# Performance work log

Measured on AMD Instinct MI355X. Metric: run time of the kernel, lower is better.

The kernel has to match this reference:

```python
import jax, jax.numpy as jnp
import numpy as np

K = 8
WRM = 40


def _gru(x, h, w_ih, w_hh, b_ih, b_hh):
    # PyTorch GRU cell: gates ordered (r, z, n)
    gi = x @ w_ih.T + b_ih
    gh = h @ w_hh.T + b_hh
    i_r, i_z, i_n = jnp.split(gi, 3, axis=-1)
    h_r, h_z, h_n = jnp.split(gh, 3, axis=-1)
    r = jax.nn.sigmoid(i_r + h_r)
    z = jax.nn.sigmoid(i_z + h_z)
    n = jnp.tanh(i_n + r * h_n)
    return (1.0 - z) * n + z * h


def setup_inputs() -> dict:
    key = jax.random.key(0)
    ks = jax.random.split(key, 20)
    T, B, C, Wd, H = 240, 64, 1, 84, 84
    N, M, E, A = 512, 256, 32, 18
    D = C * Wd * H
    u = lambda k, s, sc: jax.random.uniform(k, s, jnp.float32, -sc, sc)
    sM = float(1.0 / np.sqrt(M))
    sD = float(1.0 / np.sqrt(D))
    return dict(
        obs_seq=jax.random.normal(ks[0], (T, B, C, Wd, H), jnp.float32),
        act_seq=jax.random.randint(ks[1], (T, B), 0, A),
        w_enc=u(ks[2], (N, D), sD), b_enc=u(ks[3], (N,), sD),
        w_ih=u(ks[4], (3 * M, N), sM), w_hh=u(ks[5], (3 * M, M), sM),
        b_ih=u(ks[6], (3 * M,), sM), b_hh=u(ks[7], (3 * M,), sM),
        w_ih_c=u(ks[8], (3 * M, E), sM), w_hh_c=u(ks[9], (3 * M, M), sM),
        b_ih_c=u(ks[10], (3 * M,), sM), b_hh_c=u(ks[11], (3 * M,), sM),
        W1=u(ks[12], (M, M), sM), b1=u(ks[13], (M,), sM),
        W2=u(ks[14], (N, M), sM), b2=u(ks[15], (N,), sM),
        emb=jax.random.normal(ks[16], (A, E), jnp.float32),
    )


def reference(obs_seq, act_seq, w_enc, b_enc, w_ih, w_hh, b_ih, b_hh,
              w_ih_c, w_hh_c, b_ih_c, b_hh_c, W1, b1, W2, b2, emb):
    T, B = obs_seq.shape[0], obs_seq.shape[1]
    M = w_hh.shape[1]
    # encoder: flatten + linear -> (T, B, N)
    z = obs_seq.reshape(T, B, -1) @ w_enc.T + b_enc
    wrm_seq, trn_seq = z[:WRM], z[WRM:]
    acts = act_seq[WRM:]

    h0 = jnp.zeros((B, M), z.dtype)
    warm_hn, _ = jax.lax.scan(
        lambda h, x: (_gru(x, h, w_ih, w_hh, b_ih, b_hh), None), h0, wrm_seq)
    warm_hn = jax.lax.stop_gradient(warm_hn)  # torch.no_grad() warmup

    def cls_step(h, x):
        h2 = _gru(x, h, w_ih, w_hh, b_ih, b_hh)
        return h2, h2

    _, bts = jax.lax.scan(cls_step, warm_hn, trn_seq)  # (T', B, M)

    Tp = bts.shape[0]
    Tout = Tp - K
    idx = jnp.arange(Tout)[:, None] + jnp.arange(K)[None, :]  # (Tout, K)
    act_win = emb[acts[idx]]  # (Tout, K, B, E)

    def open_step(h, x):  # h: (Tout, B, M), x: (Tout, B, E)
        h2 = _gru(x, h, w_ih_c, w_hh_c, b_ih_c, b_hh_c)
        zt = jax.nn.relu(h2 @ W1.T + b1) @ W2.T + b2
        return h2, zt

    _, zs = jax.lax.scan(open_step, bts[:Tout], jnp.transpose(act_win, (1, 0, 2, 3)))
    return jnp.transpose(zs, (1, 0, 2, 3))  # (Tout, K, B, N)
```

## Files before the change

kernel.cpp:

```cpp
#include <hip/hip_runtime.h>
#include <hip/hip_fp16.h>
#include <math.h>

#define TT   240
#define BBATCH 64
#define DDIM 7056
#define KENC_PAD 7072
#define NENC 512
#define MHID 256
#define G3   768
#define WRMC 40
#define KWIN 8
#define TOUTC 192
#define RROWS (TOUTC*BBATCH)
#define NSTEPS (WRMC + TOUTC)

#define B_GI     ((size_t)0)
#define B_WENCH  ((size_t)0)
#define B_GBH    ((size_t)0)
#define B_R1H    ((size_t)37748736)
#define B_ZH     ((size_t)45613056)
#define B_HOPEN  ((size_t)45613056)
#define B_BTS    ((size_t)60817408)
#define B_BTSH   ((size_t)73400320)
#define B_HOPENH ((size_t)79691776)
#define B_WIHH   ((size_t)85983232)
#define B_WHHCH  ((size_t)86769664)
#define B_W1H    ((size_t)87162880)
#define B_W2H    ((size_t)87293952)
#define B_GTAB   ((size_t)87556096)
#define B_WT8    ((size_t)87611392)

typedef _Float16 half8 __attribute__((ext_vector_type(8)));
typedef _Float16 h2v  __attribute__((ext_vector_type(2)));
typedef __attribute__((ext_vector_type(4))) float f32x4;

__device__ __forceinline__ float sigmf(float x) { return 1.0f / (1.0f + expf(-x)); }
__device__ __forceinline__ h2v u2h2(unsigned int u) {
  union { unsigned int u; h2v h; } c; c.u = u; return c.h;
}

__global__ void wconv_kernel(const float* __restrict__ W, __half* __restrict__ o,
                             int N, int K, int Kpad) {
  const int idx = blockIdx.x * 256 + threadIdx.x;
  if (idx >= N * Kpad) return;
  const int n = idx / Kpad, k = idx % Kpad;
  o[idx] = __float2half((k < K) ? W[(size_t)n * K + k] : 0.f);
}

template<int AF32>
__global__ __launch_bounds__(256, 3) void gemm_hp(
    const void* __restrict__ A, const __half* __restrict__ W,
    const float* __restrict__ bias, void* __restrict__ C,
    int M, int N, int K, int Kpad, int relu, int out_h, int outk)
{
  __shared__ __half Ah[2][64][40];
  __shared__ __half Bh[2][256][40];
  const int tid = threadIdx.x;
  const int bx = blockIdx.x, by = blockIdx.y;
  const int w = tid >> 6;
  const int lane = tid & 63;
  const int l15 = lane & 15;
  const int khalf = (lane >> 4) * 8;
  const int arow = tid >> 2;
  const int akq = (tid & 3) * 8;
  const int bn = tid >> 2, bk = (tid & 3) * 8;

  f32x4 acc[4][4];
#pragma unroll
  for (int i = 0; i < 4; ++i)
#pragma unroll
    for (int j = 0; j < 4; ++j) acc[i][j] = (f32x4){0.f, 0.f, 0.f, 0.f};

  const int niter = Kpad / 32;

  float4 raA0, raA1, rahA, rbA0, rbA1, rbA2, rbA3;
  float4 raB0, raB1, rahB, rbB0, rbB1, rbB2, rbB3;

#define LOADT(IT, ra0, ra1, rah, rb0, rb1, rb2, rb3)                              \
  {                                                                               \
    const int k0_ = (IT) * 32;                                                    \
    if (AF32) {                                                                   \
      const float* Af_ = (const float*)A;                                         \
      ra0 = make_float4(0.f, 0.f, 0.f, 0.f); ra1 = ra0;                           \
      const size_t base_ = (size_t)(by * 64 + arow) * K + k0_ + akq;              \
      if (k0_ + akq < K)     ra0 = *(const float4*)(Af_ + base_);                 \
      if (k0_ + akq + 4 < K) ra1 = *(const float4*)(Af_ + base_ + 4);             \
    } else {                                                                      \
      rah = *(const float4*)((const __half*)A +                                   \
            (size_t)(by * 64 + arow) * Kpad + k0_ + akq);                         \
    }                                                                             \
    rb0 = *(const float4*)(W + (size_t)(bx * 256 + bn      ) * Kpad + k0_ + bk);  \
    rb1 = *(const float4*)(W + (size_t)(bx * 256 + bn +  64) * Kpad + k0_ + bk);  \
    rb2 = *(const float4*)(W + (size_t)(bx * 256 + bn + 128) * Kpad + k0_ + bk);  \
    rb3 = *(const float4*)(W + (size_t)(bx * 256 + bn + 192) * Kpad + k0_ + bk);  \
  }

#define BODY(IT, ra0, ra1, rah, rb0, rb1, rb2, rb3)                               \
  {                                                                               \
    __half (*Ac)[40] = Ah[(IT) & 1];                                              \
    __half (*Bc)[40] = Bh[(IT) & 1];                                              \
    if (AF32) {                                                                   \
      __half2 hh_[4];                                                             \
      hh_[0] = __floats2half2_rn(ra0.x, ra0.y);                                   \
      hh_[1] = __floats2half2_rn(ra0.z, ra0.w);                                   \
      hh_[2] = __floats2half2_rn(ra1.x, ra1.y);                                   \
      hh_[3] = __floats2half2_rn(ra1.z, ra1.w);                                   \
      *(float4*)&Ac[arow][akq] = *(float4*)hh_;                                   \
    } else {                                                                      \
      *(float4*)&Ac[arow][akq] = rah;                                             \
    }                                                                             \
    *(float4*)&Bc[bn      ][bk] = rb0;                                            \
    *(float4*)&Bc[bn +  64][bk] = rb1;                                            \
    *(float4*)&Bc[bn + 128][bk] = rb2;                                            \
    *(float4*)&Bc[bn + 192][bk] = rb3;                                            \
    __syncthreads();                                                              \
    if ((IT) + 2 < niter)                                                         \
      LOADT((IT) + 2, ra0, ra1, rah, rb0, rb1, rb2, rb3);                         \
    half8 ah_[4], bh_[4];                                                         \
    _Pragma("unroll")                                                             \
    for (int i = 0; i < 4; ++i) ah_[i] = *(half8*)&Ac[i * 16 + l15][khalf];       \
    _Pragma("unroll")                                                             \
    for (int j = 0; j < 4; ++j) bh_[j] = *(half8*)&Bc[w * 64 + j * 16 + l15][khalf]; \
    _Pragma("unroll")                                                             \
    for (int i = 0; i < 4; ++i)                                                   \
      _Pragma("unroll")                                                           \
      for (int j = 0; j < 4; ++j)                                                 \
        acc[i][j] = __builtin_amdgcn_mfma_f32_16x16x32_f16(ah_[i], bh_[j], acc[i][j], 0, 0, 0); \
  }

  LOADT(0, raA0, raA1, rahA, rbA0, rbA1, rbA2, rbA3);
  if (niter > 1) LOADT(1, raB0, raB1, rahB, rbB0, rbB1, rbB2, rbB3);

  int it = 0;
  while (true) {
    BODY(it, raA0, raA1, rahA, rbA0, rbA1, rbA2, rbA3);
    ++it; if (it == niter) break;
    BODY(it, raB0, raB1, rahB, rbB0, rbB1, rbB2, rbB3);
    ++it; if (it == niter) break;
  }
#undef BODY
#undef LOADT

  const int r4 = (lane >> 4) * 4;
#pragma unroll
  for (int j = 0; j < 4; ++j) {
    const int col = bx * 256 + w * 64 + j * 16 + l15;
    const float bc = bias ? bias[col] : 0.f;
#pragma unroll
    for (int i = 0; i < 4; ++i) {
      const int mbase = by * 64 + i * 16 + r4;
#pragma unroll
      for (int r = 0; r < 4; ++r) {
        const int m = mbase + r;
        float vv = acc[i][j][r] + bc;
        if (relu) vv = fmaxf(vv, 0.f);
        if (outk >= 0) {
          const int t = m >> 6, b = m & 63;
          ((float*)C)[(((size_t)(t * KWIN + outk) * BBATCH + b) * NENC) + col] = vv;
        } else if (out_h) {
          ((__half*)C)[(size_t)m * N + col] = __float2half(vv);
        } else {
          ((float*)C)[(size_t)m * N + col] = vv;
        }
      }
    }
  }
}

__global__ void gitab_kernel(const float* __restrict__ emb, const float* __restrict__ w_ih_c,
                             const float* __restrict__ b_ih_c, float* __restrict__ gt)
{
  const int idx = blockIdx.x * blockDim.x + threadIdx.x;
  if (idx >= 18 * G3) return;
  const int a = idx / G3, cgate = idx % G3;
  float s = b_ih_c[cgate];
#pragma unroll
  for (int e = 0; e < 32; ++e) s = fmaf(emb[a * 32 + e], w_ih_c[cgate * 32 + e], s);
  gt[idx] = s;
}

__global__ void transpose_whh_p8(const float* __restrict__ w, float4* __restrict__ wt8) {
  const int id = blockIdx.x * 256 + threadIdx.x;
  if (id >= 32 * G3) return;
  const int k8 = id / G3, j = id % G3;
  const float* src = w + (size_t)j * MHID + k8 * 8;
  __half2 h2[4];
#pragma unroll
  for (int q = 0; q < 4; ++q)
    h2[q] = __floats2half2_rn(src[2 * q], src[2 * q + 1]);
  wt8[id] = *(float4*)h2;
}

__global__ __launch_bounds__(768, 3) void scan4_kernel(
    const float* __restrict__ gi_all, const float4* __restrict__ wt8,
    const float* __restrict__ b_hh, float* __restrict__ bts,
    __half* __restrict__ bts_h)
{
  const int b = blockIdx.x;
  const int j = threadIdx.x;
  __shared__ __align__(16) float hs[256];
  __shared__ __align__(16) __half hs16[256];
  __shared__ float gacc[768];

  unsigned int wreg[128];
#pragma unroll
  for (int k8 = 0; k8 < 32; ++k8) {
    const float4 v = wt8[(size_t)k8 * G3 + j];
    const uint4 u = *(const uint4*)&v;
    wreg[k8 * 4 + 0] = u.x; wreg[k8 * 4 + 1] = u.y;
    wreg[k8 * 4 + 2] = u.z; wreg[k8 * 4 + 3] = u.w;
  }
  const float bj = b_hh[j];
  if (j < 256) { hs[j] = 0.f; hs16[j] = __float2half(0.f); }
  __syncthreads();

  const uint4* h16v = (const uint4*)hs16;

  for (int t = 0; t < NSTEPS; ++t) {
    float gr = 0.f, gz = 0.f, gn = 0.f;
    if (j < 256) {
      const float* gp = gi_all + ((size_t)t * BBATCH + b) * G3;
      gr = gp[j]; gz = gp[256 + j]; gn = gp[512 + j];
    }

    float a0 = bj, a1 = 0.f, a2 = 0.f, a3 = 0.f;
#pragma unroll
    for (int k8 = 0; k8 < 32; ++k8) {
      const uint4 hu = h16v[k8];
#if __has_builtin(__builtin_amdgcn_fdot2)
      a0 = __builtin_amdgcn_fdot2(u2h2(wreg[k8 * 4 + 0]), u2h2(hu.x), a0, false);
      a1 = __builtin_amdgcn_fdot2(u2h2(wreg[k8 * 4 + 1]), u2h2(hu.y), a1, false);
      a2 = __builtin_amdgcn_fdot2(u2h2(wreg[k8 * 4 + 2]), u2h2(hu.z), a2, false);
      a3 = __builtin_amdgcn_fdot2(u2h2(wreg[k8 * 4 + 3]), u2h2(hu.w), a3, false);
#else
      {
        const h2v w0 = u2h2(wreg[k8 * 4 + 0]), w1 = u2h2(wreg[k8 * 4 + 1]);
        const h2v w2 = u2h2(wreg[k8 * 4 + 2]), w3 = u2h2(wreg[k8 * 4 + 3]);
        const h2v x0 = u2h2(hu.x), x1 = u2h2(hu.y), x2 = u2h2(hu.z), x3 = u2h2(hu.w);
        a0 = fmaf((float)w0.x, (float)x0.x, a0); a0 = fmaf((float)w0.y, (float)x0.y, a0);
        a1 = fmaf((float)w1.x, (float)x1.x, a1); a1 = fmaf((float)w1.y, (float)x1.y, a1);
        a2 = fmaf((float)w2.x, (float)x2.x, a2); a2 = fmaf((float)w2.y, (float)x2.y, a2);
        a3 = fmaf((float)w3.x, (float)x3.x, a3); a3 = fmaf((float)w3.y, (float)x3.y, a3);
      }
#endif
    }
    gacc[j] = (a0 + a1) + (a2 + a3);
    __syncthreads();

    if (j < 256) {
      const float r = sigmf(gr + gacc[j]);
      const float z = sigmf(gz + gacc[256 + j]);
      const float n = tanhf(gn + r * gacc[512 + j]);
      const float hn = (1.f - z) * n + z * hs[j];
      hs[j] = hn;
      hs16[j] = __float2half(hn);
      if (t >= WRMC) {
        const size_t o = (((size_t)(t - WRMC)) * BBATCH + b) * MHID + j;
        bts[o] = hn;
        bts_h[o] = __float2half(hn);
      }
    }
    __syncthreads();
  }
}

__global__ __launch_bounds__(256) void open_gates(
    const float* __restrict__ gtab, const int* __restrict__ act_seq,
    const float* __restrict__ gh, const float* __restrict__ hin,
    float* __restrict__ hout, __half* __restrict__ hout_h, int kstep)
{
  const int row = blockIdx.x;
  const int j = threadIdx.x;
  const int t = row >> 6, b = row & 63;
  const int a = act_seq[(WRMC + t + kstep) * BBATCH + b];
  const float* gi = gtab + a * G3;
  const float gr = gi[j], gz = gi[256 + j], gn = gi[512 + j];
  const size_t g0 = (size_t)row * G3;
  const float hr = gh[g0 + j], hz = gh[g0 + 256 + j], hnn = gh[g0 + 512 + j];
  const float h = hin[(size_t)row * MHID + j];
  const float r = sigmf(gr + hr);
  const float z = sigmf(gz + hz);
  const float n = tanhf(gn + r * hnn);
  const float hn = (1.f - z) * n + z * h;
  hout[(size_t)row * MHID + j] = hn;
  hout_h[(size_t)row * MHID + j] = __float2half(hn);
}

extern "C" void kernel_launch(void* const* d_in, const int* in_sizes, int n_in,
                              void* d_out, int out_size, void* d_ws, size_t ws_size,
                              hipStream_t stream) {
  const float* obs    = (const float*)d_in[0];
  const int*   act    = (const int*)  d_in[1];
  const float* w_enc  = (const float*)d_in[2];
  const float* b_enc  = (const float*)d_in[3];
  const float* w_ih   = (const float*)d_in[4];
  const float* w_hh   = (const float*)d_in[5];
  const float* b_ih   = (const float*)d_in[6];
  const float* b_hh   = (const float*)d_in[7];
  const float* w_ih_c = (const float*)d_in[8];
  const float* w_hh_c = (const float*)d_in[9];
  const float* b_ih_c = (const float*)d_in[10];
  const float* b_hh_c = (const float*)d_in[11];
  const float* W1     = (const float*)d_in[12];
  const float* b1     = (const float*)d_in[13];
  const float* W2     = (const float*)d_in[14];
  const float* b2     = (const float*)d_in[15];
  const float* emb    = (const float*)d_in[16];

  char* wsb = (char*)d_ws;
  float* out = (float*)d_out;

  float*  gi      = (float*)(wsb + B_GI);
  float*  gbh     = (float*)(wsb + B_GBH);
  __half* r1_h    = (__half*)(wsb + B_R1H);
  __half* z_h     = (__half*)(wsb + B_ZH);
  float*  hopen   = (float*)(wsb + B_HOPEN);
  float*  bts     = (float*)(wsb + B_BTS);
  __half* bts_h   = (__half*)(wsb + B_BTSH);
  __half* hopen_h = (__half*)(wsb + B_HOPENH);
  __half* enc_h   = (__half*)(wsb + B_WENCH);
  __half* ih_h    = (__half*)(wsb + B_WIHH);
  __half* hhc_h   = (__half*)(wsb + B_WHHCH);
  __half* w1_h    = (__half*)(wsb + B_W1H);
  __half* w2_h    = (__half*)(wsb + B_W2H);
  float*  gtab    = (float*)(wsb + B_GTAB);
  float4* wt8     = (float4*)(wsb + B_WT8);

  const dim3 blk(256);

  wconv_kernel<<<(NENC * KENC_PAD + 255) / 256, blk, 0, stream>>>(w_enc, enc_h, NENC, DDIM, KENC_PAD);
  wconv_kernel<<<(G3 * NENC + 255) / 256, blk, 0, stream>>>(w_ih, ih_h, G3, NENC, NENC);
  wconv_kernel<<<(G3 * MHID + 255) / 256, blk, 0, stream>>>(w_hh_c, hhc_h, G3, MHID, MHID);
  wconv_kernel<<<(MHID * MHID + 255) / 256, blk, 0, stream>>>(W1, w1_h, MHID, MHID, MHID);
  wconv_kernel<<<(NENC * MHID + 255) / 256, blk, 0, stream>>>(W2, w2_h, NENC, MHID, MHID);
  gitab_kernel<<<54, 256, 0, stream>>>(emb, w_ih_c, b_ih_c, gtab);
  transpose_whh_p8<<<(32 * G3 + 255) / 256, blk, 0, stream>>>(w_hh, wt8);

  gemm_hp<1><<<dim3(NENC / 256, NSTEPS * BBATCH / 64), blk, 0, stream>>>(
      obs, enc_h, b_enc, z_h, NSTEPS * BBATCH, NENC, DDIM, KENC_PAD, 0, 1, -1);
  gemm_hp<0><<<dim3(G3 / 256, NSTEPS * BBATCH / 64), blk, 0, stream>>>(
      z_h, ih_h, b_ih, gi, NSTEPS * BBATCH, G3, NENC, NENC, 0, 0, -1);

  scan4_kernel<<<BBATCH, 768, 0, stream>>>(gi, wt8, b_hh, bts, bts_h);

  for (int k = 0; k < KWIN; ++k) {
    const __half* hin_h = (k == 0) ? bts_h : hopen_h;
    const float*  hin   = (k == 0) ? bts   : hopen;
    gemm_hp<0><<<dim3(G3 / 256, RROWS / 64), blk, 0, stream>>>(
        hin_h, hhc_h, b_hh_c, gbh, RROWS, G3, MHID, MHID, 0, 0, -1);
    open_gates<<<RROWS, 256, 0, stream>>>(gtab, act, gbh, hin, hopen, hopen_h, k);
    gemm_hp<0><<<dim3(MHID / 256, RROWS / 64), blk, 0, stream>>>(
        hopen_h, w1_h, b1, r1_h, RROWS, MHID, MHID, MHID, 1, 1, -1);
    gemm_hp<0><<<dim3(NENC / 256, RROWS / 64), blk, 0, stream>>>(
        r1_h, w2_h, b2, out, RROWS, NENC, MHID, MHID, 0, 0, k);
  }
}
```

Baseline: 1.104 ms.

## Fuse the 8-step open-loop GRU and MLP into one per-timestep kernel

Replaces the per-step sequence of four launches (hidden GEMM, gate kernel, W1 GEMM, W2 GEMM) across 8 open-loop steps with a single kernel. Each block handles one time index for all 64 batch rows and keeps hidden state in registers and LDS across the 8 steps, using MFMA directly with weights read from global memory. This removes about 32 launches and the global round-trips of gate, hidden and relu intermediates. In exchange it launches only 192 blocks of 512 threads with a large LDS footprint, rounds gate pre-activations to fp16, and rereads weights from global without LDS staging.

Result: slower. 1.384 ms (+25.3%).

```diff
diff --git a/kernel.cpp b/kernel.cpp
--- a/kernel.cpp
+++ b/kernel.cpp
@@ -17,13 +17,8 @@
 
 #define B_GI     ((size_t)0)
 #define B_WENCH  ((size_t)0)
-#define B_GBH    ((size_t)0)
-#define B_R1H    ((size_t)37748736)
 #define B_ZH     ((size_t)45613056)
-#define B_HOPEN  ((size_t)45613056)
 #define B_BTS    ((size_t)60817408)
-#define B_BTSH   ((size_t)73400320)
-#define B_HOPENH ((size_t)79691776)
 #define B_WIHH   ((size_t)85983232)
 #define B_WHHCH  ((size_t)86769664)
 #define B_W1H    ((size_t)87162880)
@@ -52,7 +47,7 @@
 __global__ __launch_bounds__(256, 3) void gemm_hp(
     const void* __restrict__ A, const __half* __restrict__ W,
     const float* __restrict__ bias, void* __restrict__ C,
-    int M, int N, int K, int Kpad, int relu, int out_h, int outk)
+    int M, int N, int K, int Kpad, int relu, int out_h)
 {
   __shared__ __half Ah[2][64][40];
   __shared__ __half Bh[2][256][40];
@@ -155,14 +150,8 @@
         const int m = mbase + r;
         float vv = acc[i][j][r] + bc;
         if (relu) vv = fmaxf(vv, 0.f);
-        if (outk >= 0) {
-          const int t = m >> 6, b = m & 63;
-          ((float*)C)[(((size_t)(t * KWIN + outk) * BBATCH + b) * NENC) + col] = vv;
-        } else if (out_h) {
-          ((__half*)C)[(size_t)m * N + col] = __float2half(vv);
-        } else {
-          ((float*)C)[(size_t)m * N + col] = vv;
-        }
+        if (out_h) ((__half*)C)[(size_t)m * N + col] = __float2half(vv);
+        else       ((float*)C)[(size_t)m * N + col] = vv;
       }
     }
   }
@@ -194,8 +183,7 @@
 
 __global__ __launch_bounds__(768, 3) void scan4_kernel(
     const float* __restrict__ gi_all, const float4* __restrict__ wt8,
-    const float* __restrict__ b_hh, float* __restrict__ bts,
-    __half* __restrict__ bts_h)
+    const float* __restrict__ b_hh, float* __restrict__ bts)
 {
   const int b = blockIdx.x;
   const int j = threadIdx.x;
@@ -255,36 +243,191 @@
       const float hn = (1.f - z) * n + z * hs[j];
       hs[j] = hn;
       hs16[j] = __float2half(hn);
-      if (t >= WRMC) {
-        const size_t o = (((size_t)(t - WRMC)) * BBATCH + b) * MHID + j;
-        bts[o] = hn;
-        bts_h[o] = __float2half(hn);
-      }
-    }
-    __syncthreads();
-  }
-}
-
-__global__ __launch_bounds__(256) void open_gates(
+      if (t >= WRMC) bts[(((size_t)(t - WRMC)) * BBATCH + b) * MHID + j] = hn;
+    }
+    __syncthreads();
+  }
+}
+
+__global__ __launch_bounds__(512, 2) void open8_kernel(
+    const float* __restrict__ bts,
+    const __half* __restrict__ whhc, const float* __restrict__ bhhc,
+    const __half* __restrict__ w1, const float* __restrict__ b1v,
+    const __half* __restrict__ w2, const float* __restrict__ b2v,
     const float* __restrict__ gtab, const int* __restrict__ act_seq,
-    const float* __restrict__ gh, const float* __restrict__ hin,
-    float* __restrict__ hout, __half* __restrict__ hout_h, int kstep)
+    float* __restrict__ out)
 {
-  const int row = blockIdx.x;
-  const int j = threadIdx.x;
-  const int t = row >> 6, b = row & 63;
-  const int a = act_seq[(WRMC + t + kstep) * BBATCH + b];
-  const float* gi = gtab + a * G3;
-  const float gr = gi[j], gz = gi[256 + j], gn = gi[512 + j];
-  const size_t g0 = (size_t)row * G3;
-  const float hr = gh[g0 + j], hz = gh[g0 + 256 + j], hnn = gh[g0 + 512 + j];
-  const float h = hin[(size_t)row * MHID + j];
-  const float r = sigmf(gr + hr);
-  const float z = sigmf(gz + hz);
-  const float n = tanhf(gn + r * hnn);
-  const float hn = (1.f - z) * n + z * h;
-  hout[(size_t)row * MHID + j] = hn;
-  hout_h[(size_t)row * MHID + j] = __float2half(hn);
+  __shared__ __align__(16) __half h16s[64][264];
+  __shared__ __align__(16) __half gbuf[768 * 68];
+  __shared__ int a_lds[64];
+
+  const int t = blockIdx.x;
+  const int tid = threadIdx.x;
+  const int w = tid >> 6;
+  const int lane = tid & 63;
+  const int l15 = lane & 15;
+  const int khalf = (lane >> 4) * 8;
+  const int r4 = (lane >> 4) * 4;
+  const int grow = tid & 63;
+  const int jb = tid >> 6;
+
+  float h32[32];
+  {
+    const float* src = bts + ((size_t)t * 64 + grow) * 256 + jb * 32;
+#pragma unroll
+    for (int q = 0; q < 8; ++q) {
+      const float4 v = *(const float4*)(src + q * 4);
+      h32[q * 4 + 0] = v.x; h32[q * 4 + 1] = v.y;
+      h32[q * 4 + 2] = v.z; h32[q * 4 + 3] = v.w;
+    }
+#pragma unroll
+    for (int q = 0; q < 4; ++q) {
+      __half2 hh[4];
+#pragma unroll
+      for (int p = 0; p < 4; ++p)
+        hh[p] = __floats2half2_rn(h32[q * 8 + p * 2], h32[q * 8 + p * 2 + 1]);
+      *(float4*)&h16s[grow][jb * 32 + q * 8] = *(float4*)hh;
+    }
+  }
+  __syncthreads();
+
+  for (int k = 0; k < KWIN; ++k) {
+    if (tid < 64) a_lds[tid] = act_seq[(WRMC + t + k) * BBATCH + tid];
+
+    f32x4 accG[4][6];
+#pragma unroll
+    for (int m = 0; m < 4; ++m)
+#pragma unroll
+      for (int c = 0; c < 6; ++c) accG[m][c] = (f32x4){0.f, 0.f, 0.f, 0.f};
+#pragma unroll
+    for (int kf = 0; kf < 8; ++kf) {
+      half8 ah[4];
+#pragma unroll
+      for (int m = 0; m < 4; ++m)
+        ah[m] = *(const half8*)&h16s[m * 16 + l15][kf * 32 + khalf];
+#pragma unroll
+      for (int c = 0; c < 6; ++c) {
+        const int col = (w * 6 + c) * 16 + l15;
+        const half8 bf = *(const half8*)(whhc + (size_t)col * 256 + kf * 32 + khalf);
+#pragma unroll
+        for (int m = 0; m < 4; ++m)
+          accG[m][c] = __builtin_amdgcn_mfma_f32_16x16x32_f16(ah[m], bf, accG[m][c], 0, 0, 0);
+      }
+    }
+#pragma unroll
+    for (int c = 0; c < 6; ++c) {
+      const int col = (w * 6 + c) * 16 + l15;
+#pragma unroll
+      for (int m = 0; m < 4; ++m) {
+        const int row0 = m * 16 + r4;
+        short4 s;
+        s.x = __half_as_short(__float2half(accG[m][c][0]));
+        s.y = __half_as_short(__float2half(accG[m][c][1]));
+        s.z = __half_as_short(__float2half(accG[m][c][2]));
+        s.w = __half_as_short(__float2half(accG[m][c][3]));
+        *(short4*)&gbuf[col * 68 + row0] = s;
+      }
+    }
+    __syncthreads();
+
+    {
+      const int a = a_lds[grow];
+      const float* gt = gtab + (size_t)a * G3;
+#pragma unroll
+      for (int i = 0; i < 32; ++i) {
+        const int col = jb * 32 + i;
+        const float ghR = __half2float(gbuf[(col)*68 + grow]);
+        const float ghZ = __half2float(gbuf[(col + 256) * 68 + grow]);
+        const float ghN = __half2float(gbuf[(col + 512) * 68 + grow]);
+        const float rr = sigmf(gt[col] + ghR + bhhc[col]);
+        const float zz = sigmf(gt[col + 256] + ghZ + bhhc[col + 256]);
+        const float nn = tanhf(gt[col + 512] + rr * (ghN + bhhc[col + 512]));
+        h32[i] = (1.f - zz) * nn + zz * h32[i];
+      }
+#pragma unroll
+      for (int q = 0; q < 4; ++q) {
+        __half2 hh[4];
+#pragma unroll
+        for (int p = 0; p < 4; ++p)
+          hh[p] = __floats2half2_rn(h32[q * 8 + p * 2], h32[q * 8 + p * 2 + 1]);
+        *(float4*)&h16s[grow][jb * 32 + q * 8] = *(float4*)hh;
+      }
+    }
+    __syncthreads();
+
+    f32x4 accT[4][2];
+#pragma unroll
+    for (int m = 0; m < 4; ++m)
+#pragma unroll
+      for (int c = 0; c < 2; ++c) accT[m][c] = (f32x4){0.f, 0.f, 0.f, 0.f};
+#pragma unroll
+    for (int kf = 0; kf < 8; ++kf) {
+      half8 ah[4];
+#pragma unroll
+      for (int m = 0; m < 4; ++m)
+        ah[m] = *(const half8*)&h16s[m * 16 + l15][kf * 32 + khalf];
+#pragma unroll
+      for (int c = 0; c < 2; ++c) {
+        const int col = (w * 2 + c) * 16 + l15;
+        const half8 bf = *(const half8*)(w1 + (size_t)col * 256 + kf * 32 + khalf);
+#pragma unroll
+        for (int m = 0; m < 4; ++m)
+          accT[m][c] = __builtin_amdgcn_mfma_f32_16x16x32_f16(ah[m], bf, accT[m][c], 0, 0, 0);
+      }
+    }
+    {
+      __half (*t1p)[264] = (__half(*)[264])gbuf;
+#pragma unroll
+      for (int c = 0; c < 2; ++c) {
+        const int col = (w * 2 + c) * 16 + l15;
+        const float bb = b1v[col];
+#pragma unroll
+        for (int m = 0; m < 4; ++m)
+#pragma unroll
+          for (int q = 0; q < 4; ++q)
+            t1p[m * 16 + r4 + q][col] = __float2half(fmaxf(accT[m][c][q] + bb, 0.f));
+      }
+    }
+    __syncthreads();
+
+    f32x4 accO[4][4];
+#pragma unroll
+    for (int m = 0; m < 4; ++m)
+#pragma unroll
+      for (int c = 0; c < 4; ++c) accO[m][c] = (f32x4){0.f, 0.f, 0.f, 0.f};
+    {
+      __half (*t1p)[264] = (__half(*)[264])gbuf;
+#pragma unroll
+      for (int kf = 0; kf < 8; ++kf) {
+        half8 ah[4];
+#pragma unroll
+        for (int m = 0; m < 4; ++m)
+          ah[m] = *(const half8*)&t1p[m * 16 + l15][kf * 32 + khalf];
+#pragma unroll
+        for (int c = 0; c < 4; ++c) {
+          const int col = (w * 4 + c) * 16 + l15;
+          const half8 bf = *(const half8*)(w2 + (size_t)col * 256 + kf * 32 + khalf);
+#pragma unroll
+          for (int m = 0; m < 4; ++m)
+            accO[m][c] = __builtin_amdgcn_mfma_f32_16x16x32_f16(ah[m], bf, accO[m][c], 0, 0, 0);
+        }
+      }
+    }
+    {
+      const size_t obase = (size_t)(t * KWIN + k) * BBATCH;
+#pragma unroll
+      for (int c = 0; c < 4; ++c) {
+        const int col = (w * 4 + c) * 16 + l15;
+        const float bb = b2v[col];
+#pragma unroll
+        for (int m = 0; m < 4; ++m)
+#pragma unroll
+          for (int q = 0; q < 4; ++q)
+            out[(obase + m * 16 + r4 + q) * NENC + col] = accO[m][c][q] + bb;
+      }
+    }
+    __syncthreads();
+  }
 }
 
 extern "C" void kernel_launch(void* const* d_in, const int* in_sizes, int n_in,
@@ -311,21 +454,16 @@
   char* wsb = (char*)d_ws;
   float* out = (float*)d_out;
 
-  float*  gi      = (float*)(wsb + B_GI);
-  float*  gbh     = (float*)(wsb + B_GBH);
-  __half* r1_h    = (__half*)(wsb + B_R1H);
-  __half* z_h     = (__half*)(wsb + B_ZH);
-  float*  hopen   = (float*)(wsb + B_HOPEN);
-  float*  bts     = (float*)(wsb + B_BTS);
-  __half* bts_h   = (__half*)(wsb + B_BTSH);
-  __half* hopen_h = (__half*)(wsb + B_HOPENH);
-  __half* enc_h   = (__half*)(wsb + B_WENCH);
-  __half* ih_h    = (__half*)(wsb + B_WIHH);
-  __half* hhc_h   = (__half*)(wsb + B_WHHCH);
-  __half* w1_h    = (__half*)(wsb + B_W1H);
-  __half* w2_h    = (__half*)(wsb + B_W2H);
-  float*  gtab    = (float*)(wsb + B_GTAB);
-  float4* wt8     = (float4*)(wsb + B_WT8);
+  float*  gi    = (float*)(wsb + B_GI);
+  __half* z_h   = (__half*)(wsb + B_ZH);
+  float*  bts   = (float*)(wsb + B_BTS);
+  __half* enc_h = (__half*)(wsb + B_WENCH);
+  __half* ih_h  = (__half*)(wsb + B_WIHH);
+  __half* hhc_h = (__half*)(wsb + B_WHHCH);
+  __half* w1_h  = (__half*)(wsb + B_W1H);
+  __half* w2_h  = (__half*)(wsb + B_W2H);
+  float*  gtab  = (float*)(wsb + B_GTAB);
+  float4* wt8   = (float4*)(wsb + B_WT8);
 
   const dim3 blk(256);
 
@@ -338,21 +476,12 @@
   transpose_whh_p8<<<(32 * G3 + 255) / 256, blk, 0, stream>>>(w_hh, wt8);
 
   gemm_hp<1><<<dim3(NENC / 256, NSTEPS * BBATCH / 64), blk, 0, stream>>>(
-      obs, enc_h, b_enc, z_h, NSTEPS * BBATCH, NENC, DDIM, KENC_PAD, 0, 1, -1);
+      obs, enc_h, b_enc, z_h, NSTEPS * BBATCH, NENC, DDIM, KENC_PAD, 0, 1);
   gemm_hp<0><<<dim3(G3 / 256, NSTEPS * BBATCH / 64), blk, 0, stream>>>(
-      z_h, ih_h, b_ih, gi, NSTEPS * BBATCH, G3, NENC, NENC, 0, 0, -1);
-
-  scan4_kernel<<<BBATCH, 768, 0, stream>>>(gi, wt8, b_hh, bts, bts_h);
-
-  for (int k = 0; k < KWIN; ++k) {
-    const __half* hin_h = (k == 0) ? bts_h : hopen_h;
-    const float*  hin   = (k == 0) ? bts   : hopen;
-    gemm_hp<0><<<dim3(G3 / 256, RROWS / 64), blk, 0, stream>>>(
-        hin_h, hhc_h, b_hh_c, gbh, RROWS, G3, MHID, MHID, 0, 0, -1);
-    open_gates<<<RROWS, 256, 0, stream>>>(gtab, act, gbh, hin, hopen, hopen_h, k);
-    gemm_hp<0><<<dim3(MHID / 256, RROWS / 64), blk, 0, stream>>>(
-        hopen_h, w1_h, b1, r1_h, RROWS, MHID, MHID, MHID, 1, 1, -1);
-    gemm_hp<0><<<dim3(NENC / 256, RROWS / 64), blk, 0, stream>>>(
-        r1_h, w2_h, b2, out, RROWS, NENC, MHID, MHID, 0, 0, k);
-  }
-}
+      z_h, ih_h, b_ih, gi, NSTEPS * BBATCH, G3, NENC, NENC, 0, 0);
+
+  scan4_kernel<<<BBATCH, 768, 0, stream>>>(gi, wt8, b_hh, bts);
+
+  open8_kernel<<<TOUTC, 512, 0, stream>>>(bts, hhc_h, b_hh_c, w1_h, b1, w2_h, b2,
+                                          gtab, act, out);
+}
```

## Compute all three GRU gates per thread in recurrent scan, double-buffer hidden state

Applied to the files above, without the earlier changes.

The recurrent scan now launches 256 threads per batch element instead of 768. Each thread keeps its r, z and n weight rows in registers (384 dwords) and computes all three gate dot products itself. This removes the shared gate-accumulator exchange and one of the two block barriers per step, and the fp32 hidden state stays in a register. A double-buffered fp16 hidden vector in shared memory replaces the old in-place update. The cost is much higher register pressure with a launch bound of one block, which risks spilling, and the fewer waves leave less latency hiding.

Result: slower. 1.416 ms (+28.2%).

```diff
diff --git a/kernel.cpp b/kernel.cpp
--- a/kernel.cpp
+++ b/kernel.cpp
@@ -38,6 +38,15 @@
 __device__ __forceinline__ float sigmf(float x) { return 1.0f / (1.0f + expf(-x)); }
 __device__ __forceinline__ h2v u2h2(unsigned int u) {
   union { unsigned int u; h2v h; } c; c.u = u; return c.h;
+}
+__device__ __forceinline__ float fdot2h(unsigned int w, unsigned int h, float acc) {
+#if __has_builtin(__builtin_amdgcn_fdot2)
+  return __builtin_amdgcn_fdot2(u2h2(w), u2h2(h), acc, false);
+#else
+  const h2v a = u2h2(w), b = u2h2(h);
+  acc = fmaf((float)a.x, (float)b.x, acc);
+  return fmaf((float)a.y, (float)b.y, acc);
+#endif
 }
 
 __global__ void wconv_kernel(const float* __restrict__ W, __half* __restrict__ o,
@@ -192,74 +201,69 @@
   wt8[id] = *(float4*)h2;
 }
 
-__global__ __launch_bounds__(768, 3) void scan4_kernel(
+__global__ __launch_bounds__(256, 1) void scan5_kernel(
     const float* __restrict__ gi_all, const float4* __restrict__ wt8,
     const float* __restrict__ b_hh, float* __restrict__ bts,
     __half* __restrict__ bts_h)
 {
   const int b = blockIdx.x;
   const int j = threadIdx.x;
-  __shared__ __align__(16) float hs[256];
-  __shared__ __align__(16) __half hs16[256];
-  __shared__ float gacc[768];
-
-  unsigned int wreg[128];
+  __shared__ __align__(16) __half hs16[2][256];
+
+  unsigned int wr_[128], wz_[128], wn_[128];
 #pragma unroll
   for (int k8 = 0; k8 < 32; ++k8) {
-    const float4 v = wt8[(size_t)k8 * G3 + j];
-    const uint4 u = *(const uint4*)&v;
-    wreg[k8 * 4 + 0] = u.x; wreg[k8 * 4 + 1] = u.y;
-    wreg[k8 * 4 + 2] = u.z; wreg[k8 * 4 + 3] = u.w;
-  }
-  const float bj = b_hh[j];
-  if (j < 256) { hs[j] = 0.f; hs16[j] = __float2half(0.f); }
+    uint4 u;
+    u = *(const uint4*)&wt8[(size_t)k8 * G3 + j];
+    wr_[k8 * 4 + 0] = u.x; wr_[k8 * 4 + 1] = u.y; wr_[k8 * 4 + 2] = u.z; wr_[k8 * 4 + 3] = u.w;
+    u = *(const uint4*)&wt8[(size_t)k8 * G3 + 256 + j];
+    wz_[k8 * 4 + 0] = u.x; wz_[k8 * 4 + 1] = u.y; wz_[k8 * 4 + 2] = u.z; wz_[k8 * 4 + 3] = u.w;
+    u = *(const uint4*)&wt8[(size_t)k8 * G3 + 512 + j];
+    wn_[k8 * 4 + 0] = u.x; wn_[k8 * 4 + 1] = u.y; wn_[k8 * 4 + 2] = u.z; wn_[k8 * 4 + 3] = u.w;
+  }
+  const float br = b_hh[j], bz = b_hh[256 + j], bnn = b_hh[512 + j];
+  float hj = 0.f;
+  hs16[0][j] = __float2half(0.f);
   __syncthreads();
 
-  const uint4* h16v = (const uint4*)hs16;
-
   for (int t = 0; t < NSTEPS; ++t) {
-    float gr = 0.f, gz = 0.f, gn = 0.f;
-    if (j < 256) {
-      const float* gp = gi_all + ((size_t)t * BBATCH + b) * G3;
-      gr = gp[j]; gz = gp[256 + j]; gn = gp[512 + j];
-    }
-
-    float a0 = bj, a1 = 0.f, a2 = 0.f, a3 = 0.f;
+    const int cur = t & 1;
+    const float* gp = gi_all + ((size_t)t * BBATCH + b) * G3;
+    const float gr = gp[j], gz = gp[256 + j], gn = gp[512 + j];
+    const uint4* h16v = (const uint4*)hs16[cur];
+
+    float r0 = br, r1 = 0.f, r2 = 0.f, r3 = 0.f;
+    float z0 = bz, z1 = 0.f, z2 = 0.f, z3 = 0.f;
+    float n0 = bnn, n1 = 0.f, n2 = 0.f, n3 = 0.f;
 #pragma unroll
     for (int k8 = 0; k8 < 32; ++k8) {
       const uint4 hu = h16v[k8];
-#if __has_builtin(__builtin_amdgcn_fdot2)
-      a0 = __builtin_amdgcn_fdot2(u2h2(wreg[k8 * 4 + 0]), u2h2(hu.x), a0, false);
-      a1 = __builtin_amdgcn_fdot2(u2h2(wreg[k8 * 4 + 1]), u2h2(hu.y), a1, false);
-      a2 = __builtin_amdgcn_fdot2(u2h2(wreg[k8 * 4 + 2]), u2h2(hu.z), a2, false);
-      a3 = __builtin_amdgcn_fdot2(u2h2(wreg[k8 * 4 + 3]), u2h2(hu.w), a3, false);
-#else
-      {
-        const h2v w0 = u2h2(wreg[k8 * 4 + 0]), w1 = u2h2(wreg[k8 * 4 + 1]);
-        const h2v w2 = u2h2(wreg[k8 * 4 + 2]), w3 = u2h2(wreg[k8 * 4 + 3]);
-        const h2v x0 = u2h2(hu.x), x1 = u2h2(hu.y), x2 = u2h2(hu.z), x3 = u2h2(hu.w);
-        a0 = fmaf((float)w0.x, (float)x0.x, a0); a0 = fmaf((float)w0.y, (float)x0.y, a0);
-        a1 = fmaf((float)w1.x, (float)x1.x, a1); a1 = fmaf((float)w1.y, (float)x1.y, a1);
-        a2 = fmaf((float)w2.x, (float)x2.x, a2); a2 = fmaf((float)w2.y, (float)x2.y, a2);
-        a3 = fmaf((float)w3.x, (float)x3.x, a3); a3 = fmaf((float)w3.y, (float)x3.y, a3);
-      }
-#endif
+      r0 = fdot2h(wr_[k8 * 4 + 0], hu.x, r0);
+      r1 = fdot2h(wr_[k8 * 4 + 1], hu.y, r1);
+      r2 = fdot2h(wr_[k8 * 4 + 2], hu.z, r2);
+      r3 = fdot2h(wr_[k8 * 4 + 3], hu.w, r3);
+      z0 = fdot2h(wz_[k8 * 4 + 0], hu.x, z0);
+      z1 = fdot2h(wz_[k8 * 4 + 1], hu.y, z1);
+      z2 = fdot2h(wz_[k8 * 4 + 2], hu.z, z2);
+      z3 = fdot2h(wz_[k8 * 4 + 3], hu.w, z3);
+      n0 = fdot2h(wn_[k8 * 4 + 0], hu.x, n0);
+      n1 = fdot2h(wn_[k8 * 4 + 1], hu.y, n1);
+      n2 = fdot2h(wn_[k8 * 4 + 2], hu.z, n2);
+      n3 = fdot2h(wn_[k8 * 4 + 3], hu.w, n3);
     }
-    gacc[j] = (a0 + a1) + (a2 + a3);
-    __syncthreads();
-
-    if (j < 256) {
-      const float r = sigmf(gr + gacc[j]);
-      const float z = sigmf(gz + gacc[256 + j]);
-      const float n = tanhf(gn + r * gacc[512 + j]);
-      const float hn = (1.f - z) * n + z * hs[j];
-      hs[j] = hn;
-      hs16[j] = __float2half(hn);
-      if (t >= WRMC) {
-        const size_t o = (((size_t)(t - WRMC)) * BBATCH + b) * MHID + j;
-        bts[o] = hn;
-        bts_h[o] = __float2half(hn);
-      }
+    const float accr = (r0 + r1) + (r2 + r3);
+    const float accz = (z0 + z1) + (z2 + z3);
+    const float accn = (n0 + n1) + (n2 + n3);
+    const float r = sigmf(gr + accr);
+    const float z = sigmf(gz + accz);
+    const float n = tanhf(gn + r * accn);
+    hj = (1.f - z) * n + z * hj;
+
+    hs16[cur ^ 1][j] = __float2half(hj);
+    if (t >= WRMC) {
+      const size_t o = (((size_t)(t - WRMC)) * BBATCH + b) * MHID + j;
+      bts[o] = hj;
+      bts_h[o] = __float2half(hj);
     }
     __syncthreads();
   }
@@ -342,7 +346,7 @@
   gemm_hp<0><<<dim3(G3 / 256, NSTEPS * BBATCH / 64), blk, 0, stream>>>(
       z_h, ih_h, b_ih, gi, NSTEPS * BBATCH, G3, NENC, NENC, 0, 0, -1);
 
-  scan4_kernel<<<BBATCH, 768, 0, stream>>>(gi, wt8, b_hh, bts, bts_h);
+  scan5_kernel<<<BBATCH, 256, 0, stream>>>(gi, wt8, b_hh, bts, bts_h);
 
   for (int k = 0; k < KWIN; ++k) {
     const __half* hin_h = (k == 0) ? bts_h : hopen_h;
```
